# Optimization experiments

Hardware: AMD Instinct MI355X
Metric: run time of the kernel (lower is better)

The kernel has to match this reference:

```python
import jax, jax.numpy as jnp
import numpy as np

EPS = 1e-5
K = 9
DILATION = 1

def bn(x, g, b, m, v):
    # x: (B,C,N,1), inference-mode BatchNorm2d with running stats
    sh = (1, -1, 1, 1)
    return (x - m.reshape(sh)) * (g.reshape(sh) / jnp.sqrt(v.reshape(sh) + EPS)) + b.reshape(sh)

def conv1x1(x, w, b):
    # w: (Cout, Cin), x: (B,Cin,N,1)
    return jnp.einsum('oc,bcnj->bonj', w, x) + b.reshape(1, -1, 1, 1)

def knn_idx(feat, k):
    # feat: (B,C,N) -> (B,N,k) indices of k nearest nodes (incl. self)
    xt = jnp.transpose(feat, (0, 2, 1))  # (B,N,C)
    x2 = jnp.sum(xt * xt, axis=-1)       # (B,N)
    dist = x2[:, :, None] - 2.0 * jnp.einsum('bnc,bmc->bnm', xt, xt) + x2[:, None, :]
    _, idx = jax.lax.top_k(-dist, k)
    return idx

def setup_inputs():
    key = jax.random.key(0)
    ks = jax.random.split(key, 24)
    B, C, H, W = 16, 256, 32, 32
    HID = 512
    def g(i, shape, s=1.0):
        return jax.random.normal(ks[i], shape, dtype=jnp.float32) * s
    def pos(i, shape):
        return jax.random.uniform(ks[i], shape, dtype=jnp.float32, minval=0.5, maxval=1.5)
    return {
        'x': g(0, (B, C, H, W)),
        'fc1_w': g(1, (C, C), 0.05), 'fc1_b': g(2, (C,), 0.05),
        'bn1_g': pos(3, (C,)), 'bn1_b': g(4, (C,), 0.1), 'bn1_m': g(5, (C,), 0.1), 'bn1_v': pos(6, (C,)),
        'gc_w': g(7, (HID, 2 * C), 0.05), 'gc_b': g(8, (HID,), 0.05),
        'gbn_g': pos(9, (HID,)), 'gbn_b': g(10, (HID,), 0.1), 'gbn_m': g(11, (HID,), 0.1), 'gbn_v': pos(12, (HID,)),
        'bn2_g': pos(13, (HID,)), 'bn2_b': g(14, (HID,), 0.1), 'bn2_m': g(15, (HID,), 0.1), 'bn2_v': pos(16, (HID,)),
        'fc2_w': g(17, (C, HID), 0.05), 'fc2_b': g(18, (C,), 0.05),
        'bn3_g': pos(19, (C,)), 'bn3_b': g(20, (C,), 0.1), 'bn3_m': g(21, (C,), 0.1), 'bn3_v': pos(22, (C,)),
    }

def reference(x, fc1_w, fc1_b, bn1_g, bn1_b, bn1_m, bn1_v,
              gc_w, gc_b, gbn_g, gbn_b, gbn_m, gbn_v,
              bn2_g, bn2_b, bn2_m, bn2_v,
              fc2_w, fc2_b, bn3_g, bn3_b, bn3_m, bn3_v):
    B, C, H, W = x.shape
    N = H * W
    x = x.reshape(B, C, N, 1)
    shortcut = x
    # fc1: 1x1 conv + BN
    h = bn(conv1x1(x, fc1_w, fc1_b), bn1_g, bn1_b, bn1_m, bn1_v)
    # DyGraphConv2d: dynamic dilated kNN graph over N nodes
    feat = h[..., 0]  # (B,C,N)
    idx = knn_idx(feat, K * DILATION)[:, :, ::DILATION]  # (B,N,K)
    # MRConv2d: max over neighbors of (x_j - x_i)
    x_j = jax.vmap(lambda f, i: f[:, i])(feat, idx)        # (B,C,N,K) gather
    diff_max = jnp.max(x_j - feat[:, :, :, None], axis=-1)  # (B,C,N)
    # interleave [x, max_diff] along channel dim -> (B, 2C, N, 1)
    m = jnp.stack([feat, diff_max], axis=2).reshape(B, 2 * C, N, 1)
    g = conv1x1(m, gc_w, gc_b)
    g = bn(g, gbn_g, gbn_b, gbn_m, gbn_v)  # BasicConv BN, act='None'
    # graph_conv Sequential: BN + GELU (erf, torch default)
    g = jax.nn.gelu(bn(g, bn2_g, bn2_b, bn2_m, bn2_v), approximate=False)
    # fc2 + residual (drop_path=0 -> identity)
    out = bn(conv1x1(g, fc2_w, fc2_b), bn3_g, bn3_b, bn3_m, bn3_v)
    return out + shortcut
```

## Files before the change

### kernel.cpp

```cpp
#include <hip/hip_runtime.h>
#include <hip/hip_bf16.h>
#include <stdint.h>

typedef unsigned long long u64;
typedef __hip_bfloat16 bf16;
typedef short s8v __attribute__((ext_vector_type(8)));
typedef short s4v __attribute__((ext_vector_type(4)));
typedef float f4v __attribute__((ext_vector_type(4)));

#define B_   16
#define C_   256
#define N_   1024
#define HID_ 512

__device__ __forceinline__ unsigned short f2b(float f) {
    unsigned u = __float_as_uint(f);
    unsigned r = (u + 0x7FFFu + ((u >> 16) & 1u)) >> 16;
    return (unsigned short)r;
}
__device__ __forceinline__ float b2f(unsigned short s) {
    return __uint_as_float(((unsigned)s) << 16);
}
__device__ __forceinline__ float ldIn(const void* p, long long i, int bf) {
    return bf ? b2f(((const unsigned short*)p)[i]) : ((const float*)p)[i];
}
__device__ __forceinline__ u64 shfl_xor_u64(u64 v, int m) {
    unsigned lo = (unsigned)v, hi = (unsigned)(v >> 32);
    lo = __shfl_xor(lo, m, 64);
    hi = __shfl_xor(hi, m, 64);
    return ((u64)hi << 32) | lo;
}

__global__ void prep_kernel(const void* xp,
    const void* fc1_b, const void* bn1_g, const void* bn1_b, const void* bn1_m, const void* bn1_v,
    const void* gc_b,  const void* gbn_g, const void* gbn_b, const void* gbn_m, const void* gbn_v,
    const void* bn2_g, const void* bn2_b, const void* bn2_m, const void* bn2_v,
    const void* fc2_b, const void* bn3_g, const void* bn3_b, const void* bn3_m, const void* bn3_v,
    int* flags, float* s1, float* t1, float* Sg, float* Tg, float* s3, float* t3,
    float* x2)
{
    __shared__ int sf;
    if (threadIdx.x == 0) {
        const unsigned short* u = (const unsigned short*)xp;
        int cnt = 0;
        for (int i = 0; i < 64; ++i) {
            int e = (u[2 * i] >> 7) & 0xFF;
            cnt += (e >= 87 && e <= 167);
        }
        int f = (cnt >= 48) ? 1 : 0;
        flags[0] = f;
        sf = f;
    }
    for (int i = threadIdx.x; i < B_ * N_; i += 512) x2[i] = 0.f;
    __syncthreads();
    int bf = sf;
    int i = threadIdx.x;
    if (i < 256) {
        float g = ldIn(bn1_g, i, bf), bb = ldIn(bn1_b, i, bf);
        float m = ldIn(bn1_m, i, bf), v  = ldIn(bn1_v, i, bf);
        float s = g / sqrtf(v + 1e-5f);
        s1[i] = s;
        t1[i] = (ldIn(fc1_b, i, bf) - m) * s + bb;

        float g3 = ldIn(bn3_g, i, bf), b3 = ldIn(bn3_b, i, bf);
        float m3 = ldIn(bn3_m, i, bf), v3 = ldIn(bn3_v, i, bf);
        float ss3 = g3 / sqrtf(v3 + 1e-5f);
        s3[i] = ss3;
        t3[i] = (ldIn(fc2_b, i, bf) - m3) * ss3 + b3;
    }
    if (i < 512) {
        float gg = ldIn(gbn_g, i, bf), gb = ldIn(gbn_b, i, bf);
        float gm = ldIn(gbn_m, i, bf), gv = ldIn(gbn_v, i, bf);
        float sg = gg / sqrtf(gv + 1e-5f);
        float g2 = ldIn(bn2_g, i, bf), b2 = ldIn(bn2_b, i, bf);
        float m2 = ldIn(bn2_m, i, bf), v2 = ldIn(bn2_v, i, bf);
        float s2 = g2 / sqrtf(v2 + 1e-5f);
        Sg[i] = sg * s2;
        Tg[i] = ((ldIn(gc_b, i, bf) - gm) * sg + gb - m2) * s2 + b2;
    }
}

__global__ __launch_bounds__(256)
void cast_weights(const void* w1, const void* wg, const void* w2,
                  short* W1b, short* Wgb, short* W2b, const int* flags)
{
    int inf = flags[0];
    int i = blockIdx.x * 256 + threadIdx.x;
    if (i < 65536) {
        W1b[i] = (short)f2b(ldIn(w1, i, inf));
    } else if (i < 65536 + 262144) {
        int j = i - 65536;
        Wgb[j] = (short)f2b(ldIn(wg, j, inf));
    } else {
        int j = i - 327680;
        W2b[j] = (short)f2b(ldIn(w2, j, inf));
    }
}

__global__ __launch_bounds__(256)
void fc1_valu(const void* __restrict__ Aw, const void* __restrict__ Bx,
              float* __restrict__ Ft, short* __restrict__ Fhi,
              short* __restrict__ Flo, float* __restrict__ x2,
              const float* __restrict__ s1, const float* __restrict__ t1,
              const int* __restrict__ flags)
{
    __shared__ float As[16][68];
    __shared__ float Bs[16][68];
    __shared__ float x2part[16][64];

    int inf = flags[0];
    int b  = blockIdx.z;
    int o0 = blockIdx.y * 64, n0 = blockIdx.x * 64;
    int t  = threadIdx.x;
    int tn = t & 15, to = t >> 4;
    long long bbase = (long long)b * C_ * N_;

    float acc[4][4] = {};

    for (int k0 = 0; k0 < C_; k0 += 16) {
        {
            int l = t * 4;
            int ao = l >> 4, ak = l & 15;
            long long ai = (long long)(o0 + ao) * C_ + k0 + ak;
            As[ak + 0][ao] = ldIn(Aw, ai + 0, inf);
            As[ak + 1][ao] = ldIn(Aw, ai + 1, inf);
            As[ak + 2][ao] = ldIn(Aw, ai + 2, inf);
            As[ak + 3][ao] = ldIn(Aw, ai + 3, inf);
        }
        {
            int l = t * 4;
            int bk = l >> 6, bn = l & 63;
            long long bi = bbase + (long long)(k0 + bk) * N_ + n0 + bn;
            Bs[bk][bn + 0] = ldIn(Bx, bi + 0, inf);
            Bs[bk][bn + 1] = ldIn(Bx, bi + 1, inf);
            Bs[bk][bn + 2] = ldIn(Bx, bi + 2, inf);
            Bs[bk][bn + 3] = ldIn(Bx, bi + 3, inf);
        }
        __syncthreads();
        #pragma unroll
        for (int k = 0; k < 16; ++k) {
            float av[4], bv[4];
            #pragma unroll
            for (int i = 0; i < 4; ++i) av[i] = As[k][to * 4 + i];
            #pragma unroll
            for (int j = 0; j < 4; ++j) bv[j] = Bs[k][tn * 4 + j];
            #pragma unroll
            for (int i = 0; i < 4; ++i)
                #pragma unroll
                for (int j = 0; j < 4; ++j) acc[i][j] += av[i] * bv[j];
        }
        __syncthreads();
    }

    float p2[4] = {};
    #pragma unroll
    for (int i = 0; i < 4; ++i) {
        int o = o0 + to * 4 + i;
        float s = s1[o], tt = t1[o];
        #pragma unroll
        for (int j = 0; j < 4; ++j) {
            int n = n0 + tn * 4 + j;
            float f = acc[i][j] * s + tt;
            long long oi = ((long long)(b << 10) + n) * C_ + o;
            Ft[oi] = f;
            unsigned short h = f2b(f);
            Fhi[oi] = (short)h;
            Flo[oi] = (short)f2b(f - b2f(h));
            p2[j] += f * f;
        }
    }
    #pragma unroll
    for (int j = 0; j < 4; ++j) x2part[to][tn * 4 + j] = p2[j];
    __syncthreads();
    if (t < 64) {
        float s = 0.f;
        #pragma unroll
        for (int r = 0; r < 16; ++r) s += x2part[r][t];
        atomicAdd(&x2[(b << 10) + n0 + t], s);
    }
}

__global__ __launch_bounds__(256)
void gram_topk(const short* __restrict__ Fhi, const short* __restrict__ Flo,
               const float* __restrict__ x2, u64* __restrict__ Part)
{
    __shared__ __align__(16) char ldsbuf[31232];
    short* Ah  = (short*)(ldsbuf);
    short* Al  = (short*)(ldsbuf + 10240);
    short* Bh  = (short*)(ldsbuf + 20480);
    short* Bl  = (short*)(ldsbuf + 25600);
    float* x2s = (float*)(ldsbuf + 30720);
    u64*   mrg  = (u64*)(ldsbuf);
    u64*   mrg2 = (u64*)(ldsbuf + 20480);

    int t = threadIdx.x;
    int q0 = blockIdx.x * 64, mq = blockIdx.y, b = blockIdx.z;
    int wv = t >> 6, ln15 = t & 15, quad = (t >> 4) & 3;

    if (t < 128) x2s[t] = x2[(b << 10) + mq * 128 + t];

    f4v acc[8];
    #pragma unroll
    for (int i = 0; i < 8; ++i) acc[i] = 0.f;

    for (int kc = 0; kc < 8; ++kc) {
        __syncthreads();
        #pragma unroll
        for (int s = 0; s < 6; ++s) {
            int sid = t + s * 256;
            int row = sid >> 2, seg = sid & 3;
            const short* src;
            short* dst;
            int grow;
            if (row < 128)      { dst = &Ah[row * 40 + seg * 8];         grow = mq * 128 + row;       src = Fhi; }
            else if (row < 256) { dst = &Al[(row - 128) * 40 + seg * 8]; grow = mq * 128 + row - 128; src = Flo; }
            else if (row < 320) { dst = &Bh[(row - 256) * 40 + seg * 8]; grow = q0 + row - 256;       src = Fhi; }
            else                { dst = &Bl[(row - 320) * 40 + seg * 8]; grow = q0 + row - 320;       src = Flo; }
            *(s8v*)dst = *(const s8v*)(src + ((long long)((b << 10) + grow)) * C_ + kc * 32 + seg * 8);
        }
        __syncthreads();
        s8v qh = *(s8v*)&Bh[(wv * 16 + ln15) * 40 + quad * 8];
        s8v ql = *(s8v*)&Bl[(wv * 16 + ln15) * 40 + quad * 8];
        #pragma unroll
        for (int i = 0; i < 8; ++i) {
            s8v mh = *(s8v*)&Ah[(i * 16 + ln15) * 40 + quad * 8];
            s8v ml = *(s8v*)&Al[(i * 16 + ln15) * 40 + quad * 8];
            acc[i] = __builtin_amdgcn_mfma_f32_16x16x32_bf16(mh, qh, acc[i], 0, 0, 0);
            acc[i] = __builtin_amdgcn_mfma_f32_16x16x32_bf16(mh, ql, acc[i], 0, 0, 0);
            acc[i] = __builtin_amdgcn_mfma_f32_16x16x32_bf16(ml, qh, acc[i], 0, 0, 0);
        }
    }

    u64 l[9];
    #pragma unroll
    for (int i = 0; i < 9; ++i) l[i] = ~0ULL;
    #pragma unroll
    for (int i = 0; i < 8; ++i) {
        #pragma unroll
        for (int r = 0; r < 4; ++r) {
            int mloc = i * 16 + quad * 4 + r;
            float d = x2s[mloc] - 2.f * acc[i][r];
            unsigned u = __float_as_uint(d);
            u = (u & 0x80000000u) ? ~u : (u | 0x80000000u);
            u64 key = ((u64)u << 32) | (unsigned)(mq * 128 + mloc);
            if (key < l[8]) {
                u64 x = key;
                #pragma unroll
                for (int jj = 0; jj < 9; ++jj) {
                    u64 lo2 = l[jj] < x ? l[jj] : x;
                    u64 hi2 = l[jj] < x ? x : l[jj];
                    l[jj] = lo2; x = hi2;
                }
            }
        }
    }

    __syncthreads();
    {
        int qloc = wv * 16 + ln15;
        #pragma unroll
        for (int k = 0; k < 9; ++k) mrg[(qloc * 4 + quad) * 9 + k] = l[k];
    }
    __syncthreads();
    if (t < 128) {
        int r = t >> 1, pr = t & 1;
        const u64* LA = &mrg[(r * 4 + pr * 2) * 9];
        const u64* LB = LA + 9;
        int ia = 0, ib = 0;
        u64* Po = &mrg2[(r * 2 + pr) * 9];
        #pragma unroll
        for (int k = 0; k < 9; ++k) {
            u64 va = LA[ia], vb = LB[ib];
            bool ta = va < vb;
            Po[k] = ta ? va : vb;
            ia += ta; ib += !ta;
        }
    }
    __syncthreads();
    if (t < 64) {
        const u64* LA = &mrg2[(t * 2) * 9];
        const u64* LB = LA + 9;
        int ia = 0, ib = 0;
        u64* P = Part + (((long long)((b << 10) + q0 + t)) * 8 + mq) * 9;
        #pragma unroll
        for (int k = 0; k < 9; ++k) {
            u64 va = LA[ia], vb = LB[ib];
            bool ta = va < vb;
            P[k] = ta ? va : vb;
            ia += ta; ib += !ta;
        }
    }
}

__global__ __launch_bounds__(256)
void build_Mt(const float* __restrict__ Ft, const u64* __restrict__ Part,
              short* __restrict__ Mt)
{
    int t = threadIdx.x;
    int wv = t >> 6, lane = t & 63;
    int n = blockIdx.x * 4 + wv;
    int b = blockIdx.y;
    long long nb = (long long)(b << 10) + n;

    const u64* L = Part + nb * 72 + (long long)(lane & 7) * 9;
    u64 l[9];
    #pragma unroll
    for (int k = 0; k < 9; ++k) l[k] = L[k];
    #pragma unroll
    for (int s = 1; s <= 4; s <<= 1) {
        u64 p[9];
        #pragma unroll
        for (int k = 0; k < 9; ++k) p[k] = shfl_xor_u64(l[k], s);
        #pragma unroll
        for (int k = 0; k < 9; ++k) {
            u64 x = p[k];
            if (x < l[8]) {
                #pragma unroll
                for (int jj = 0; jj < 9; ++jj) {
                    u64 lo2 = l[jj] < x ? l[jj] : x;
                    u64 hi2 = l[jj] < x ? x : l[jj];
                    l[jj] = lo2; x = hi2;
                }
            }
        }
    }

    int c0 = lane * 4;
    f4v f = *(const f4v*)(Ft + nb * C_ + c0);
    f4v mx = {-3.4e38f, -3.4e38f, -3.4e38f, -3.4e38f};
    #pragma unroll
    for (int k = 0; k < 9; ++k) {
        int id = (int)(l[k] & 0xFFFFFFFFu);
        f4v g = *(const f4v*)(Ft + ((long long)(b << 10) + id) * C_ + c0);
        mx[0] = fmaxf(mx[0], g[0]); mx[1] = fmaxf(mx[1], g[1]);
        mx[2] = fmaxf(mx[2], g[2]); mx[3] = fmaxf(mx[3], g[3]);
    }
    s8v m8;
    #pragma unroll
    for (int r = 0; r < 4; ++r) {
        m8[2 * r]     = (short)f2b(f[r]);
        m8[2 * r + 1] = (short)f2b(mx[r] - f[r]);
    }
    *(s8v*)(Mt + nb * (2 * C_) + 2 * c0) = m8;
}

template<int EPI>
__global__ __launch_bounds__(256)
void mfma_gemm(const short* __restrict__ A, const short* __restrict__ Bm,
               void* __restrict__ Out, const float* __restrict__ scale,
               const float* __restrict__ bias, const void* __restrict__ resid,
               const int* __restrict__ flags, int K, int Odim)
{
    __shared__ short As[128][40];
    __shared__ short Bs[128][40];

    int t = threadIdx.x, b = blockIdx.z;
    int n0 = blockIdx.x * 128, o0 = blockIdx.y * 128;
    int wv = t >> 6, ln = t & 15, quad = (t >> 4) & 3;
    int wo = (wv & 1) * 64, wn = (wv >> 1) * 64;

    f4v acc[4][4];
    #pragma unroll
    for (int i = 0; i < 4; ++i)
        #pragma unroll
        for (int j = 0; j < 4; ++j) acc[i][j] = 0.f;

    const short* Ab = A + (long long)o0 * K;
    const short* Bb = Bm + ((long long)(b << 10) + n0) * K;

    for (int k0 = 0; k0 < K; k0 += 32) {
        __syncthreads();
        #pragma unroll
        for (int s = 0; s < 2; ++s) {
            int sid = t + s * 256;
            int row = sid >> 2, seg = sid & 3;
            *(s8v*)&As[row][seg * 8] = *(const s8v*)(Ab + (long long)row * K + k0 + seg * 8);
            *(s8v*)&Bs[row][seg * 8] = *(const s8v*)(Bb + (long long)row * K + k0 + seg * 8);
        }
        __syncthreads();
        s8v a[4], bf[4];
        #pragma unroll
        for (int i = 0; i < 4; ++i) a[i]  = *(s8v*)&As[wo + i * 16 + ln][quad * 8];
        #pragma unroll
        for (int j = 0; j < 4; ++j) bf[j] = *(s8v*)&Bs[wn + j * 16 + ln][quad * 8];
        #pragma unroll
        for (int i = 0; i < 4; ++i)
            #pragma unroll
            for (int j = 0; j < 4; ++j)
                acc[i][j] = __builtin_amdgcn_mfma_f32_16x16x32_bf16(a[i], bf[j], acc[i][j], 0, 0, 0);
    }

    int inf = flags[0];
    #pragma unroll
    for (int i = 0; i < 4; ++i) {
        int ob = o0 + wo + i * 16 + quad * 4;
        #pragma unroll
        for (int j = 0; j < 4; ++j) {
            int n = n0 + wn + j * 16 + ln;
            f4v v = acc[i][j];
            if (EPI == 0) {
                s4v g;
                #pragma unroll
                for (int r = 0; r < 4; ++r) {
                    float val = v[r] * scale[ob + r] + bias[ob + r];
                    val = 0.5f * val * (1.0f + erff(val * 0.70710678118654752f));
                    g[r] = (short)f2b(val);
                }
                *(s4v*)((short*)Out + ((long long)(b << 10) + n) * Odim + ob) = g;
            } else {
                #pragma unroll
                for (int r = 0; r < 4; ++r) {
                    int o = ob + r;
                    long long oi = ((long long)b * Odim + o) * N_ + n;
                    ((float*)Out)[oi] = v[r] * scale[o] + bias[o] + ldIn(resid, oi, inf);
                }
            }
        }
    }
}

extern "C" void kernel_launch(void* const* d_in, const int* in_sizes, int n_in,
                              void* d_out, int out_size, void* d_ws, size_t ws_size,
                              hipStream_t stream)
{
    const void* p[23];
    if (n_in >= 23 && in_sizes[0] != 4194304 && in_sizes[22] == 4194304) {
        const int amap[23] = {
            22, 13, 12, 1, 0, 2, 3,
            21, 20, 17, 16, 18, 19,
            5, 4, 6, 7,
            15, 14, 9, 8, 10, 11 };
        for (int i = 0; i < 23; ++i) p[i] = d_in[amap[i]];
    } else {
        for (int i = 0; i < 23; ++i) p[i] = d_in[i];
    }

    const void* x     = p[0];
    const void* fc1_w = p[1];
    const void* fc1_b = p[2];
    const void* bn1_g = p[3];
    const void* bn1_b = p[4];
    const void* bn1_m = p[5];
    const void* bn1_v = p[6];
    const void* gc_w  = p[7];
    const void* gc_b  = p[8];
    const void* gbn_g = p[9];
    const void* gbn_b = p[10];
    const void* gbn_m = p[11];
    const void* gbn_v = p[12];
    const void* bn2_g = p[13];
    const void* bn2_b = p[14];
    const void* bn2_m = p[15];
    const void* bn2_v = p[16];
    const void* fc2_w = p[17];
    const void* fc2_b = p[18];
    const void* bn3_g = p[19];
    const void* bn3_b = p[20];
    const void* bn3_m = p[21];
    const void* bn3_v = p[22];

    char* ws = (char*)d_ws;
    size_t off = 0;
    int*   flags = (int*)ws;
    float* s1 = (float*)(ws + 256);
    float* t1 = s1 + 256;
    float* s3 = t1 + 256;
    float* t3 = s3 + 256;
    float* Sg = t3 + 256;
    float* Tg = Sg + 512;
    off = 16384;
    short* W1b   = (short*)(ws + off); off += (size_t)C_ * C_ * 2;
    short* Wgb   = (short*)(ws + off); off += (size_t)HID_ * 2 * C_ * 2;
    short* W2b   = (short*)(ws + off); off += (size_t)C_ * HID_ * 2;
    float* Ft    = (float*)(ws + off); off += (size_t)B_ * N_ * C_ * 4;
    short* Fhi   = (short*)(ws + off); off += (size_t)B_ * N_ * C_ * 2;
    short* Flo   = (short*)(ws + off); off += (size_t)B_ * N_ * C_ * 2;
    float* x2    = (float*)(ws + off); off += (size_t)B_ * N_ * 4;
    u64*   Part  = (u64*)  (ws + off); off += (size_t)B_ * N_ * 8 * 9 * 8;
    short* Mt    = (short*)(ws + off); off += (size_t)B_ * N_ * 2 * C_ * 2;
    short* Gt    = (short*)(ws + off); off += (size_t)B_ * N_ * HID_ * 2;

    prep_kernel<<<1, 512, 0, stream>>>(x,
        fc1_b, bn1_g, bn1_b, bn1_m, bn1_v,
        gc_b, gbn_g, gbn_b, gbn_m, gbn_v,
        bn2_g, bn2_b, bn2_m, bn2_v,
        fc2_b, bn3_g, bn3_b, bn3_m, bn3_v,
        flags, s1, t1, Sg, Tg, s3, t3, x2);

    cast_weights<<<1792, 256, 0, stream>>>(fc1_w, gc_w, fc2_w,
                                           W1b, Wgb, W2b, flags);

    fc1_valu<<<dim3(16, 4, B_), 256, 0, stream>>>(
        fc1_w, x, Ft, Fhi, Flo, x2, s1, t1, flags);

    gram_topk<<<dim3(16, 8, 16), 256, 0, stream>>>(Fhi, Flo, x2, Part);

    build_Mt<<<dim3(256, 16), 256, 0, stream>>>(Ft, Part, Mt);

    mfma_gemm<0><<<dim3(8, 4, 16), 256, 0, stream>>>(
        Wgb, Mt, Gt, Sg, Tg, nullptr, flags, 2 * C_, HID_);

    mfma_gemm<1><<<dim3(8, 2, 16), 256, 0, stream>>>(
        W2b, Gt, d_out, s3, t3, x, flags, HID_, C_);
}
```

Before: 336.6 us.

## Move fc1 to split-bf16 MFMA and retile downstream GEMMs to 128x64

Replaces the fp32 VALU fc1 GEMM with an MFMA kernel that keeps near-fp32 accuracy through a hi/lo bf16 split (three MFMAs per tile). A new transpose kernel pre-splits x into node-major hi/lo bf16, and the weight cast also emits a lo part. The two later MFMA GEMMs change from 128x128 to 128x64 tiles, doubling the grid so more blocks fill the CUs. This costs an extra transpose pass, more workspace, and three times the MFMA work for fc1.

```diff
diff --git a/kernel.cpp b/kernel.cpp
--- a/kernel.cpp
+++ b/kernel.cpp
@@ -82,12 +82,16 @@
 
 __global__ __launch_bounds__(256)
 void cast_weights(const void* w1, const void* wg, const void* w2,
-                  short* W1b, short* Wgb, short* W2b, const int* flags)
+                  short* W1h, short* W1l, short* Wgb, short* W2b,
+                  const int* flags)
 {
     int inf = flags[0];
     int i = blockIdx.x * 256 + threadIdx.x;
     if (i < 65536) {
-        W1b[i] = (short)f2b(ldIn(w1, i, inf));
+        float f = ldIn(w1, i, inf);
+        unsigned short h = f2b(f);
+        W1h[i] = (short)h;
+        W1l[i] = (short)f2b(f - b2f(h));
     } else if (i < 65536 + 262144) {
         int j = i - 65536;
         Wgb[j] = (short)f2b(ldIn(wg, j, inf));
@@ -98,86 +102,122 @@
 }
 
 __global__ __launch_bounds__(256)
-void fc1_valu(const void* __restrict__ Aw, const void* __restrict__ Bx,
+void transpose_split_x(const void* __restrict__ X, short* __restrict__ xth,
+                       short* __restrict__ xtl, const int* __restrict__ flags)
+{
+    __shared__ float tile[64][68];
+    int inf = flags[0];
+    int t = threadIdx.x;
+    int n0 = blockIdx.x * 64, c0 = blockIdx.y * 64, b = blockIdx.z;
+
+    #pragma unroll
+    for (int rr = 0; rr < 4; ++rr) {
+        int cl = (t >> 4) + rr * 16;
+        int nl = (t & 15) * 4;
+        long long g = ((long long)b * C_ + c0 + cl) * N_ + n0 + nl;
+        if (inf) {
+            s4v v = *(const s4v*)((const short*)X + g);
+            tile[cl][nl + 0] = b2f((unsigned short)v[0]);
+            tile[cl][nl + 1] = b2f((unsigned short)v[1]);
+            tile[cl][nl + 2] = b2f((unsigned short)v[2]);
+            tile[cl][nl + 3] = b2f((unsigned short)v[3]);
+        } else {
+            f4v v = *(const f4v*)((const float*)X + g);
+            tile[cl][nl + 0] = v[0]; tile[cl][nl + 1] = v[1];
+            tile[cl][nl + 2] = v[2]; tile[cl][nl + 3] = v[3];
+        }
+    }
+    __syncthreads();
+
+    int nl = t >> 2, cseg = t & 3;
+    long long base = ((long long)((b << 10) + n0 + nl)) * C_ + c0 + cseg * 16;
+    s8v h0, h1, l0, l1;
+    #pragma unroll
+    for (int cc = 0; cc < 16; ++cc) {
+        float f = tile[cseg * 16 + cc][nl];
+        unsigned short h = f2b(f);
+        unsigned short l = f2b(f - b2f(h));
+        if (cc < 8) { h0[cc] = (short)h; l0[cc] = (short)l; }
+        else        { h1[cc - 8] = (short)h; l1[cc - 8] = (short)l; }
+    }
+    *(s8v*)(xth + base)     = h0;
+    *(s8v*)(xth + base + 8) = h1;
+    *(s8v*)(xtl + base)     = l0;
+    *(s8v*)(xtl + base + 8) = l1;
+}
+
+__global__ __launch_bounds__(256)
+void fc1_mfma(const short* __restrict__ W1h, const short* __restrict__ W1l,
+              const short* __restrict__ xth, const short* __restrict__ xtl,
+              const float* __restrict__ s1, const float* __restrict__ t1,
               float* __restrict__ Ft, short* __restrict__ Fhi,
-              short* __restrict__ Flo, float* __restrict__ x2,
-              const float* __restrict__ s1, const float* __restrict__ t1,
-              const int* __restrict__ flags)
-{
-    __shared__ float As[16][68];
-    __shared__ float Bs[16][68];
-    __shared__ float x2part[16][64];
-
-    int inf = flags[0];
-    int b  = blockIdx.z;
-    int o0 = blockIdx.y * 64, n0 = blockIdx.x * 64;
-    int t  = threadIdx.x;
-    int tn = t & 15, to = t >> 4;
-    long long bbase = (long long)b * C_ * N_;
-
-    float acc[4][4] = {};
-
-    for (int k0 = 0; k0 < C_; k0 += 16) {
-        {
-            int l = t * 4;
-            int ao = l >> 4, ak = l & 15;
-            long long ai = (long long)(o0 + ao) * C_ + k0 + ak;
-            As[ak + 0][ao] = ldIn(Aw, ai + 0, inf);
-            As[ak + 1][ao] = ldIn(Aw, ai + 1, inf);
-            As[ak + 2][ao] = ldIn(Aw, ai + 2, inf);
-            As[ak + 3][ao] = ldIn(Aw, ai + 3, inf);
-        }
-        {
-            int l = t * 4;
-            int bk = l >> 6, bn = l & 63;
-            long long bi = bbase + (long long)(k0 + bk) * N_ + n0 + bn;
-            Bs[bk][bn + 0] = ldIn(Bx, bi + 0, inf);
-            Bs[bk][bn + 1] = ldIn(Bx, bi + 1, inf);
-            Bs[bk][bn + 2] = ldIn(Bx, bi + 2, inf);
-            Bs[bk][bn + 3] = ldIn(Bx, bi + 3, inf);
-        }
+              short* __restrict__ Flo, float* __restrict__ x2)
+{
+    __shared__ __align__(16) char ldsbuf[30720];
+    short* Wh = (short*)(ldsbuf);
+    short* Wl = (short*)(ldsbuf + 10240);
+    short* Xh = (short*)(ldsbuf + 20480);
+    short* Xl = (short*)(ldsbuf + 25600);
+
+    int t = threadIdx.x;
+    int n0 = blockIdx.x * 64, o0 = blockIdx.y * 128, b = blockIdx.z;
+    int wv = t >> 6, ln15 = t & 15, quad = (t >> 4) & 3;
+
+    f4v acc[8];
+    #pragma unroll
+    for (int i = 0; i < 8; ++i) acc[i] = 0.f;
+
+    for (int kc = 0; kc < 8; ++kc) {
         __syncthreads();
         #pragma unroll
-        for (int k = 0; k < 16; ++k) {
-            float av[4], bv[4];
-            #pragma unroll
-            for (int i = 0; i < 4; ++i) av[i] = As[k][to * 4 + i];
-            #pragma unroll
-            for (int j = 0; j < 4; ++j) bv[j] = Bs[k][tn * 4 + j];
-            #pragma unroll
-            for (int i = 0; i < 4; ++i)
-                #pragma unroll
-                for (int j = 0; j < 4; ++j) acc[i][j] += av[i] * bv[j];
+        for (int s = 0; s < 6; ++s) {
+            int sid = t + s * 256;
+            int row = sid >> 2, seg = sid & 3;
+            const short* src;
+            short* dst;
+            if (row < 128)      { dst = &Wh[row * 40 + seg * 8];         src = W1h + (long long)(o0 + row) * C_; }
+            else if (row < 256) { dst = &Wl[(row - 128) * 40 + seg * 8]; src = W1l + (long long)(o0 + row - 128) * C_; }
+            else if (row < 320) { dst = &Xh[(row - 256) * 40 + seg * 8]; src = xth + ((long long)((b << 10) + n0 + row - 256)) * C_; }
+            else                { dst = &Xl[(row - 320) * 40 + seg * 8]; src = xtl + ((long long)((b << 10) + n0 + row - 320)) * C_; }
+            *(s8v*)dst = *(const s8v*)(src + kc * 32 + seg * 8);
         }
         __syncthreads();
-    }
-
-    float p2[4] = {};
-    #pragma unroll
-    for (int i = 0; i < 4; ++i) {
-        int o = o0 + to * 4 + i;
-        float s = s1[o], tt = t1[o];
-        #pragma unroll
-        for (int j = 0; j < 4; ++j) {
-            int n = n0 + tn * 4 + j;
-            float f = acc[i][j] * s + tt;
-            long long oi = ((long long)(b << 10) + n) * C_ + o;
-            Ft[oi] = f;
-            unsigned short h = f2b(f);
-            Fhi[oi] = (short)h;
-            Flo[oi] = (short)f2b(f - b2f(h));
-            p2[j] += f * f;
-        }
-    }
-    #pragma unroll
-    for (int j = 0; j < 4; ++j) x2part[to][tn * 4 + j] = p2[j];
-    __syncthreads();
-    if (t < 64) {
-        float s = 0.f;
-        #pragma unroll
-        for (int r = 0; r < 16; ++r) s += x2part[r][t];
-        atomicAdd(&x2[(b << 10) + n0 + t], s);
-    }
+        s8v xh8 = *(s8v*)&Xh[(wv * 16 + ln15) * 40 + quad * 8];
+        s8v xl8 = *(s8v*)&Xl[(wv * 16 + ln15) * 40 + quad * 8];
+        #pragma unroll
+        for (int i = 0; i < 8; ++i) {
+            s8v wh8 = *(s8v*)&Wh[(i * 16 + ln15) * 40 + quad * 8];
+            s8v wl8 = *(s8v*)&Wl[(i * 16 + ln15) * 40 + quad * 8];
+            acc[i] = __builtin_amdgcn_mfma_f32_16x16x32_bf16(wh8, xh8, acc[i], 0, 0, 0);
+            acc[i] = __builtin_amdgcn_mfma_f32_16x16x32_bf16(wh8, xl8, acc[i], 0, 0, 0);
+            acc[i] = __builtin_amdgcn_mfma_f32_16x16x32_bf16(wl8, xh8, acc[i], 0, 0, 0);
+        }
+    }
+
+    int n = n0 + wv * 16 + ln15;
+    long long nb = (long long)(b << 10) + n;
+    float p2 = 0.f;
+    #pragma unroll
+    for (int i = 0; i < 8; ++i) {
+        int ob = o0 + i * 16 + quad * 4;
+        f4v f;
+        s4v hi, lo;
+        #pragma unroll
+        for (int r = 0; r < 4; ++r) {
+            float v = acc[i][r] * s1[ob + r] + t1[ob + r];
+            f[r] = v;
+            unsigned short h = f2b(v);
+            hi[r] = (short)h;
+            lo[r] = (short)f2b(v - b2f(h));
+            p2 += v * v;
+        }
+        *(f4v*)(Ft  + nb * C_ + ob) = f;
+        *(s4v*)(Fhi + nb * C_ + ob) = hi;
+        *(s4v*)(Flo + nb * C_ + ob) = lo;
+    }
+    p2 += __shfl_xor(p2, 16, 64);
+    p2 += __shfl_xor(p2, 32, 64);
+    if (quad == 0) atomicAdd(&x2[nb], p2);
 }
 
 __global__ __launch_bounds__(256)
@@ -351,69 +391,60 @@
                const float* __restrict__ bias, const void* __restrict__ resid,
                const int* __restrict__ flags, int K, int Odim)
 {
-    __shared__ short As[128][40];
-    __shared__ short Bs[128][40];
+    __shared__ __align__(16) short As[128 * 40];
+    __shared__ __align__(16) short Bs[64 * 40];
 
     int t = threadIdx.x, b = blockIdx.z;
-    int n0 = blockIdx.x * 128, o0 = blockIdx.y * 128;
-    int wv = t >> 6, ln = t & 15, quad = (t >> 4) & 3;
-    int wo = (wv & 1) * 64, wn = (wv >> 1) * 64;
-
-    f4v acc[4][4];
-    #pragma unroll
-    for (int i = 0; i < 4; ++i)
-        #pragma unroll
-        for (int j = 0; j < 4; ++j) acc[i][j] = 0.f;
-
-    const short* Ab = A + (long long)o0 * K;
-    const short* Bb = Bm + ((long long)(b << 10) + n0) * K;
-
-    for (int k0 = 0; k0 < K; k0 += 32) {
+    int n0 = blockIdx.x * 64, o0 = blockIdx.y * 128;
+    int wv = t >> 6, ln15 = t & 15, quad = (t >> 4) & 3;
+
+    f4v acc[8];
+    #pragma unroll
+    for (int i = 0; i < 8; ++i) acc[i] = 0.f;
+
+    int nkc = K >> 5;
+    for (int kc = 0; kc < nkc; ++kc) {
         __syncthreads();
         #pragma unroll
-        for (int s = 0; s < 2; ++s) {
+        for (int s = 0; s < 3; ++s) {
             int sid = t + s * 256;
             int row = sid >> 2, seg = sid & 3;
-            *(s8v*)&As[row][seg * 8] = *(const s8v*)(Ab + (long long)row * K + k0 + seg * 8);
-            *(s8v*)&Bs[row][seg * 8] = *(const s8v*)(Bb + (long long)row * K + k0 + seg * 8);
+            if (row < 128)
+                *(s8v*)&As[row * 40 + seg * 8] =
+                    *(const s8v*)(A + (long long)(o0 + row) * K + kc * 32 + seg * 8);
+            else
+                *(s8v*)&Bs[(row - 128) * 40 + seg * 8] =
+                    *(const s8v*)(Bm + ((long long)((b << 10) + n0 + row - 128)) * K + kc * 32 + seg * 8);
         }
         __syncthreads();
-        s8v a[4], bf[4];
-        #pragma unroll
-        for (int i = 0; i < 4; ++i) a[i]  = *(s8v*)&As[wo + i * 16 + ln][quad * 8];
-        #pragma unroll
-        for (int j = 0; j < 4; ++j) bf[j] = *(s8v*)&Bs[wn + j * 16 + ln][quad * 8];
-        #pragma unroll
-        for (int i = 0; i < 4; ++i)
+        s8v bf = *(s8v*)&Bs[(wv * 16 + ln15) * 40 + quad * 8];
+        #pragma unroll
+        for (int i = 0; i < 8; ++i) {
+            s8v a = *(s8v*)&As[(i * 16 + ln15) * 40 + quad * 8];
+            acc[i] = __builtin_amdgcn_mfma_f32_16x16x32_bf16(a, bf, acc[i], 0, 0, 0);
+        }
+    }
+
+    int inf = flags[0];
+    int n = n0 + wv * 16 + ln15;
+    #pragma unroll
+    for (int i = 0; i < 8; ++i) {
+        int ob = o0 + i * 16 + quad * 4;
+        if (EPI == 0) {
+            s4v g;
             #pragma unroll
-            for (int j = 0; j < 4; ++j)
-                acc[i][j] = __builtin_amdgcn_mfma_f32_16x16x32_bf16(a[i], bf[j], acc[i][j], 0, 0, 0);
-    }
-
-    int inf = flags[0];
-    #pragma unroll
-    for (int i = 0; i < 4; ++i) {
-        int ob = o0 + wo + i * 16 + quad * 4;
-        #pragma unroll
-        for (int j = 0; j < 4; ++j) {
-            int n = n0 + wn + j * 16 + ln;
-            f4v v = acc[i][j];
-            if (EPI == 0) {
-                s4v g;
-                #pragma unroll
-                for (int r = 0; r < 4; ++r) {
-                    float val = v[r] * scale[ob + r] + bias[ob + r];
-                    val = 0.5f * val * (1.0f + erff(val * 0.70710678118654752f));
-                    g[r] = (short)f2b(val);
-                }
-                *(s4v*)((short*)Out + ((long long)(b << 10) + n) * Odim + ob) = g;
-            } else {
-                #pragma unroll
-                for (int r = 0; r < 4; ++r) {
-                    int o = ob + r;
-                    long long oi = ((long long)b * Odim + o) * N_ + n;
-                    ((float*)Out)[oi] = v[r] * scale[o] + bias[o] + ldIn(resid, oi, inf);
-                }
+            for (int r = 0; r < 4; ++r) {
+                float val = acc[i][r] * scale[ob + r] + bias[ob + r];
+                val = 0.5f * val * (1.0f + erff(val * 0.70710678118654752f));
+                g[r] = (short)f2b(val);
+            }
+            *(s4v*)((short*)Out + ((long long)((b << 10) + n)) * Odim + ob) = g;
+        } else {
+            #pragma unroll
+            for (int r = 0; r < 4; ++r) {
+                int o = ob + r;
+                long long oi = ((long long)b * Odim + o) * N_ + n;
+                ((float*)Out)[oi] = acc[i][r] * scale[o] + bias[o] + ldIn(resid, oi, inf);
             }
         }
     }
@@ -469,9 +500,12 @@
     float* Sg = t3 + 256;
     float* Tg = Sg + 512;
     off = 16384;
-    short* W1b   = (short*)(ws + off); off += (size_t)C_ * C_ * 2;
+    short* W1h   = (short*)(ws + off); off += (size_t)C_ * C_ * 2;
+    short* W1l   = (short*)(ws + off); off += (size_t)C_ * C_ * 2;
     short* Wgb   = (short*)(ws + off); off += (size_t)HID_ * 2 * C_ * 2;
     short* W2b   = (short*)(ws + off); off += (size_t)C_ * HID_ * 2;
+    short* xth   = (short*)(ws + off); off += (size_t)B_ * N_ * C_ * 2;
+    short* xtl   = (short*)(ws + off); off += (size_t)B_ * N_ * C_ * 2;
     float* Ft    = (float*)(ws + off); off += (size_t)B_ * N_ * C_ * 4;
     short* Fhi   = (short*)(ws + off); off += (size_t)B_ * N_ * C_ * 2;
     short* Flo   = (short*)(ws + off); off += (size_t)B_ * N_ * C_ * 2;
@@ -488,18 +522,20 @@
         flags, s1, t1, Sg, Tg, s3, t3, x2);
 
     cast_weights<<<1792, 256, 0, stream>>>(fc1_w, gc_w, fc2_w,
-                                           W1b, Wgb, W2b, flags);
-
-    fc1_valu<<<dim3(16, 4, B_), 256, 0, stream>>>(
-        fc1_w, x, Ft, Fhi, Flo, x2, s1, t1, flags);
+                                           W1h, W1l, Wgb, W2b, flags);
+
+    transpose_split_x<<<dim3(16, 4, 16), 256, 0, stream>>>(x, xth, xtl, flags);
+
+    fc1_mfma<<<dim3(16, 2, 16), 256, 0, stream>>>(
+        W1h, W1l, xth, xtl, s1, t1, Ft, Fhi, Flo, x2);
 
     gram_topk<<<dim3(16, 8, 16), 256, 0, stream>>>(Fhi, Flo, x2, Part);
 
     build_Mt<<<dim3(256, 16), 256, 0, stream>>>(Ft, Part, Mt);
 
-    mfma_gemm<0><<<dim3(8, 4, 16), 256, 0, stream>>>(
+    mfma_gemm<0><<<dim3(16, 4, 16), 256, 0, stream>>>(
         Wgb, Mt, Gt, Sg, Tg, nullptr, flags, 2 * C_, HID_);
 
-    mfma_gemm<1><<<dim3(8, 2, 16), 256, 0, stream>>>(
+    mfma_gemm<1><<<dim3(16, 2, 16), 256, 0, stream>>>(
         W2b, Gt, d_out, s3, t3, x, flags, HID_, C_);
 }
```

Result: faster. 304.4 us (-9.6%).
